# Kernel optimization log

Hardware: AMD Instinct MI355X
Metric: run time of the kernel (lower is better)

## Reference

```python
import jax, jax.numpy as jnp
import numpy as np

D_MODEL = 1024
NUM_HEADS = 16
B, S = 1, 4096


def setup_inputs() -> dict:
    key = jax.random.key(0)
    kx, kq, kk, kv, ko = jax.random.split(key, 5)
    std = (1.0 / D_MODEL) ** 0.5
    def trunc(k):
        return std * jax.random.truncated_normal(k, -3.0, 3.0, (D_MODEL, D_MODEL), dtype=jnp.float32)
    return {
        "x": jax.random.normal(kx, (B, S, D_MODEL), dtype=jnp.float32),
        "W_Q": trunc(kq),
        "W_K": trunc(kk),
        "W_V": trunc(kv),
        "W_O": trunc(ko),
    }


def reference(x, W_Q, W_K, W_V, W_O):
    Bx, Sx, Dm = x.shape
    H = NUM_HEADS
    d_attn = Dm // H
    # projections (torch code uses x @ W.T)
    Q = x @ W_Q.T
    K = x @ W_K.T
    V = x @ W_V.T
    # [B, H, S, d]
    Q = Q.reshape(Bx, Sx, H, d_attn).transpose(0, 2, 1, 3)
    K = K.reshape(Bx, Sx, H, d_attn).transpose(0, 2, 1, 3)
    V = V.reshape(Bx, Sx, H, d_attn).transpose(0, 2, 1, 3)
    scale = 1.0 / jnp.sqrt(jnp.asarray(d_attn, dtype=x.dtype))
    # [B, H, S, S] scores
    attn = jnp.einsum("bhqd,bhkd->bhqk", Q, K) * scale
    causal = jnp.tril(jnp.ones((Sx, Sx), dtype=bool))
    attn = jnp.where(causal, attn, jnp.asarray(-jnp.inf, dtype=attn.dtype))
    probs = jax.nn.softmax(attn, axis=-1)
    y = jnp.einsum("bhqk,bhkd->bhqd", probs, V)
    y = y.transpose(0, 2, 1, 3).reshape(Bx, Sx, Dm)
    return y @ W_O.T
```

## Files before the change

### kernel.cpp

```cpp
#include <hip/hip_runtime.h>

#define S_LEN 4096
#define DMODEL 1024
#define NHEADS 16

typedef __attribute__((ext_vector_type(8))) short bf16x8;
typedef __attribute__((ext_vector_type(4))) float f32x4;
typedef unsigned short u16;
typedef unsigned int u32;
typedef unsigned long long u64;

__device__ inline u16 f2bf(float f) {
    union { float f; u32 u; } v; v.f = f;
    u32 r = v.u + 0x7fffu + ((v.u >> 16) & 1u);
    return (u16)(r >> 16);
}

__device__ inline u32 pkbf2(float a, float b) {
    union { float f; u32 u; } ua, ub; ua.f = a; ub.f = b;
    const u32 ra = ua.u + 0x7fffu + ((ua.u >> 16) & 1u);
    const u32 rb = ub.u + 0x7fffu + ((ub.u >> 16) & 1u);
    return __builtin_amdgcn_perm(rb, ra, 0x07060302u);
}

__device__ inline void cp16(const void* g, void* l) {
    __builtin_amdgcn_global_load_lds(
        (const __attribute__((address_space(1))) unsigned int*)g,
        (__attribute__((address_space(3))) unsigned int*)l, 16, 0, 0);
}

__global__ __launch_bounds__(256) void cvt_all(const float* __restrict__ x,
                                               const float* __restrict__ wq,
                                               const float* __restrict__ wk,
                                               const float* __restrict__ wv,
                                               const float* __restrict__ wo,
                                               u16* __restrict__ xb,
                                               u16* __restrict__ w3,
                                               u16* __restrict__ wob) {
    const int b = blockIdx.x;
    const float* s; u16* d; int off;
    const int NW = DMODEL * DMODEL;
    if (b < 2048)      { s = x;  d = xb;          off = b * 2048; }
    else if (b < 2560) { s = wq; d = w3;          off = (b - 2048) * 2048; }
    else if (b < 3072) { s = wk; d = w3 + NW;     off = (b - 2560) * 2048; }
    else if (b < 3584) { s = wv; d = w3 + 2 * NW; off = (b - 3072) * 2048; }
    else               { s = wo; d = wob;         off = (b - 3584) * 2048; }
    const int i = off + threadIdx.x * 8;
    const float4 a = *(const float4*)(s + i);
    const float4 c = *(const float4*)(s + i + 4);
    u16 t[8];
    t[0] = f2bf(a.x); t[1] = f2bf(a.y); t[2] = f2bf(a.z); t[3] = f2bf(a.w);
    t[4] = f2bf(c.x); t[5] = f2bf(c.y); t[6] = f2bf(c.z); t[7] = f2bf(c.w);
    *(bf16x8*)(d + i) = *(const bf16x8*)t;
}

__global__ __launch_bounds__(256) void gemm_qkv(const u16* __restrict__ A,
                                                const u16* __restrict__ B3,
                                                u16* __restrict__ Qo,
                                                u16* __restrict__ Ko,
                                                u16* __restrict__ Vo) {
    __shared__ __align__(16) u16 As[2][128 * 32];
    __shared__ __align__(16) u16 Bs[2][128 * 32];
    const int tid = threadIdx.x, lane = tid & 63, wave = tid >> 6;
    const int wm = (wave >> 1) * 64, wn = (wave & 1) * 64;
    const int m0 = blockIdx.y * 128, n0 = blockIdx.x * 128;
    const int l15 = lane & 15, quad = lane >> 4;

    f32x4 acc[4][4];
#pragma unroll
    for (int i = 0; i < 4; i++)
#pragma unroll
        for (int j = 0; j < 4; j++) acc[i][j] = (f32x4){0.f, 0.f, 0.f, 0.f};

    const int r0 = tid >> 2, c0 = (tid & 3) * 8;

    cp16(A + (size_t)(m0 + r0) * 1024 + c0,       As[0] + r0 * 32 + c0);
    cp16(A + (size_t)(m0 + r0 + 64) * 1024 + c0,  As[0] + (r0 + 64) * 32 + c0);
    cp16(B3 + (size_t)(n0 + r0) * 1024 + c0,      Bs[0] + r0 * 32 + c0);
    cp16(B3 + (size_t)(n0 + r0 + 64) * 1024 + c0, Bs[0] + (r0 + 64) * 32 + c0);

    int cur = 0;
    for (int kk = 0; kk < 1024; kk += 32) {
        __syncthreads();
        if (kk + 32 < 1024) {
            const int kn = kk + 32;
            cp16(A + (size_t)(m0 + r0) * 1024 + kn + c0,       As[cur ^ 1] + r0 * 32 + c0);
            cp16(A + (size_t)(m0 + r0 + 64) * 1024 + kn + c0,  As[cur ^ 1] + (r0 + 64) * 32 + c0);
            cp16(B3 + (size_t)(n0 + r0) * 1024 + kn + c0,      Bs[cur ^ 1] + r0 * 32 + c0);
            cp16(B3 + (size_t)(n0 + r0 + 64) * 1024 + kn + c0, Bs[cur ^ 1] + (r0 + 64) * 32 + c0);
        }
        bf16x8 af[4], bfr[4];
#pragma unroll
        for (int i = 0; i < 4; i++)
            af[i] = *(const bf16x8*)(As[cur] + (wm + i * 16 + l15) * 32 + quad * 8);
#pragma unroll
        for (int j = 0; j < 4; j++)
            bfr[j] = *(const bf16x8*)(Bs[cur] + (wn + j * 16 + l15) * 32 + quad * 8);
#pragma unroll
        for (int i = 0; i < 4; i++)
#pragma unroll
            for (int j = 0; j < 4; j++)
                acc[i][j] = __builtin_amdgcn_mfma_f32_16x16x32_bf16(af[i], bfr[j], acc[i][j], 0, 0, 0);
        cur ^= 1;
    }

    const int which = n0 >> 10;
    const int n0r = n0 & 1023;
    u16* dst = (which == 0) ? Qo : (which == 1) ? Ko : Vo;
    const float sc = (which == 0) ? 0.125f * 1.4426950408889634f : 1.0f;
#pragma unroll
    for (int i = 0; i < 4; i++)
#pragma unroll
        for (int j = 0; j < 4; j++)
#pragma unroll
            for (int r = 0; r < 4; r++) {
                const int row = m0 + wm + i * 16 + quad * 4 + r;
                const int col = n0r + wn + j * 16 + l15;
                const int h = col >> 6, c = col & 63;
                const u16 v = f2bf(acc[i][j][r] * sc);
                if (which < 2) dst[(size_t)h * S_LEN * 64 + (size_t)row * 64 + c] = v;
                else           dst[(size_t)h * S_LEN * 64 + (size_t)c * S_LEN + row] = v;
            }
}

__global__ __launch_bounds__(256) void gemm_out(const u16* __restrict__ A,
                                                const u16* __restrict__ B,
                                                float* __restrict__ C) {
    __shared__ __align__(16) u16 As[2][64 * 64];
    __shared__ __align__(16) u16 Bs[2][128 * 64];
    const int tid = threadIdx.x, lane = tid & 63, wave = tid >> 6;
    const int wm = (wave >> 1) * 32, wn = (wave & 1) * 64;
    const int bx = blockIdx.x;
    const int n0 = (bx & 7) * 128, m0 = (bx >> 3) * 64;
    const int l15 = lane & 15, quad = lane >> 4;
    const int swz = l15 & 7;

    f32x4 acc[2][4];
#pragma unroll
    for (int i = 0; i < 2; i++)
#pragma unroll
        for (int j = 0; j < 4; j++) acc[i][j] = (f32x4){0.f, 0.f, 0.f, 0.f};

#define STAGE_OUT(buf, kb)                                                              \
    {                                                                                   \
        _Pragma("unroll")                                                               \
        for (int q = 0; q < 2; q++) {                                                   \
            const int ch = tid + q * 256;                                               \
            const int ar = ch >> 3, ac = ((ch & 7) ^ (ar & 7)) * 8;                     \
            cp16(A + (size_t)(m0 + ar) * 1024 + (kb) + ac, As[buf] + ch * 8);           \
        }                                                                               \
        _Pragma("unroll")                                                               \
        for (int q = 0; q < 4; q++) {                                                   \
            const int ch = tid + q * 256;                                               \
            const int br = ch >> 3, bc = ((ch & 7) ^ (br & 7)) * 8;                     \
            cp16(B + (size_t)(n0 + br) * 1024 + (kb) + bc, Bs[buf] + ch * 8);           \
        }                                                                               \
    }

    STAGE_OUT(0, 0);
    int cur = 0;
    for (int kk = 0; kk < 1024; kk += 64) {
        __syncthreads();
        if (kk + 64 < 1024) STAGE_OUT(cur ^ 1, kk + 64);
#pragma unroll
        for (int h = 0; h < 2; h++) {
            const int cc = (h * 4 + quad) ^ swz;
            bf16x8 af[2], bfr[4];
#pragma unroll
            for (int i = 0; i < 2; i++)
                af[i] = *(const bf16x8*)(As[cur] + (wm + i * 16 + l15) * 64 + cc * 8);
#pragma unroll
            for (int j = 0; j < 4; j++)
                bfr[j] = *(const bf16x8*)(Bs[cur] + (wn + j * 16 + l15) * 64 + cc * 8);
#pragma unroll
            for (int i = 0; i < 2; i++)
#pragma unroll
                for (int j = 0; j < 4; j++)
                    acc[i][j] = __builtin_amdgcn_mfma_f32_16x16x32_bf16(af[i], bfr[j], acc[i][j], 0, 0, 0);
        }
        cur ^= 1;
    }
#undef STAGE_OUT

#pragma unroll
    for (int i = 0; i < 2; i++)
#pragma unroll
        for (int j = 0; j < 4; j++)
#pragma unroll
            for (int r = 0; r < 4; r++) {
                const int row = m0 + wm + i * 16 + quad * 4 + r;
                const int col = n0 + wn + j * 16 + l15;
                C[(size_t)row * 1024 + col] = acc[i][j][r];
            }
}

__global__ __launch_bounds__(256) void attn(const u16* __restrict__ Q,
                                            const u16* __restrict__ Kh,
                                            const u16* __restrict__ Vt,
                                            u16* __restrict__ Y) {
    __shared__ __align__(16) u16 Ks[2][64 * 64];
    __shared__ __align__(16) u16 Vs[2][64 * 64];
    __shared__ __align__(16) u16 Pl[4][32 * 72];
    const int b = blockIdx.x;
    const int head = b & 15;
    const int bb = b >> 4;
    const int j = (b < 256) ? bb : 47 - bb;
    const int qaA = 64 * j;
    const int qaB = 64 * (63 - j);
    const int nktB = 64 - j;
    const int tid = threadIdx.x, lane = tid & 63, w = tid >> 6;
    const int l15 = lane & 15, quad = lane >> 4;
    const int swz = l15 & 7;

    const u16* Qp = Q + (size_t)head * S_LEN * 64;
    const u16* Kp = Kh + (size_t)head * S_LEN * 64;
    const u16* Vp = Vt + (size_t)head * 64 * S_LEN;

    const int qrowA = qaA + w * 16 + l15;
    const int qrowB = qaB + w * 16 + l15;
    const int srow = tid >> 3;
    const int scol = ((tid & 7) ^ (srow & 7)) * 8;

    bf16x8 aq[2][2];
#pragma unroll
    for (int s = 0; s < 2; s++) {
        aq[0][s] = *(const bf16x8*)(Qp + (size_t)qrowA * 64 + s * 32 + quad * 8);
        aq[1][s] = *(const bf16x8*)(Qp + (size_t)qrowB * 64 + s * 32 + quad * 8);
    }

    f32x4 o[2][4];
#pragma unroll
    for (int g = 0; g < 2; g++)
#pragma unroll
        for (int jj = 0; jj < 4; jj++) o[g][jj] = (f32x4){0.f, 0.f, 0.f, 0.f};
    float lrow[2] = {0.f, 0.f};

    cp16(Kp + (size_t)srow * 64 + scol,        Ks[0] + tid * 8);
    cp16(Kp + (size_t)(srow + 32) * 64 + scol, Ks[0] + tid * 8 + 2048);
    cp16(Vp + (size_t)srow * S_LEN + scol,        Vs[0] + tid * 8);
    cp16(Vp + (size_t)(srow + 32) * S_LEN + scol, Vs[0] + tid * 8 + 2048);

    int cur = 0;
    for (int kt = 0; kt < nktB; kt++) {
        __syncthreads();
        if (kt + 1 < nktB) {
            const int kn = (kt + 1) * 64;
            cp16(Kp + (size_t)(kn + srow) * 64 + scol,      Ks[cur ^ 1] + tid * 8);
            cp16(Kp + (size_t)(kn + srow + 32) * 64 + scol, Ks[cur ^ 1] + tid * 8 + 2048);
            cp16(Vp + (size_t)srow * S_LEN + kn + scol,        Vs[cur ^ 1] + tid * 8);
            cp16(Vp + (size_t)(srow + 32) * S_LEN + kn + scol, Vs[cur ^ 1] + tid * 8 + 2048);
        }
        const u16* K_ = Ks[cur];
        const u16* V_ = Vs[cur];
        const int kb = kt * 64;
        const bool actA = (kt <= j);
        const bool bndA = (kt == j);
        const bool bndB = (kt == nktB - 1);
#pragma unroll
        for (int t = 0; t < 4; t++) {
            const bf16x8 k0 = *(const bf16x8*)(K_ + (t * 16 + l15) * 64 + (quad ^ swz) * 8);
            const bf16x8 k1 = *(const bf16x8*)(K_ + (t * 16 + l15) * 64 + ((4 + quad) ^ swz) * 8);
            const int keyb = kb + t * 16 + quad * 4;
            {
                f32x4 c = (f32x4){0.f, 0.f, 0.f, 0.f};
                c = __builtin_amdgcn_mfma_f32_16x16x32_bf16(k0, aq[1][0], c, 0, 0, 0);
                c = __builtin_amdgcn_mfma_f32_16x16x32_bf16(k1, aq[1][1], c, 0, 0, 0);
                float p[4];
#pragma unroll
                for (int r = 0; r < 4; r++) {
                    p[r] = exp2f(c[r]);
                    if (bndB && (keyb + r > qrowB)) p[r] = 0.f;
                }
                lrow[1] += (p[0] + p[1]) + (p[2] + p[3]);
                const u32 w0 = pkbf2(p[0], p[1]);
                const u32 w1 = pkbf2(p[2], p[3]);
                *(u64*)(&Pl[w][(16 + l15) * 72 + t * 16 + quad * 4]) =
                    (u64)w0 | ((u64)w1 << 32);
            }
            if (actA) {
                f32x4 c = (f32x4){0.f, 0.f, 0.f, 0.f};
                c = __builtin_amdgcn_mfma_f32_16x16x32_bf16(k0, aq[0][0], c, 0, 0, 0);
                c = __builtin_amdgcn_mfma_f32_16x16x32_bf16(k1, aq[0][1], c, 0, 0, 0);
                float p[4];
#pragma unroll
                for (int r = 0; r < 4; r++) {
                    p[r] = exp2f(c[r]);
                    if (bndA && (keyb + r > qrowA)) p[r] = 0.f;
                }
                lrow[0] += (p[0] + p[1]) + (p[2] + p[3]);
                const u32 w0 = pkbf2(p[0], p[1]);
                const u32 w1 = pkbf2(p[2], p[3]);
                *(u64*)(&Pl[w][l15 * 72 + t * 16 + quad * 4]) =
                    (u64)w0 | ((u64)w1 << 32);
            }
        }
        bf16x8 pB0, pB1, pA0, pA1;
        pB0 = *(const bf16x8*)(&Pl[w][(16 + l15) * 72 + quad * 8]);
        pB1 = *(const bf16x8*)(&Pl[w][(16 + l15) * 72 + 32 + quad * 8]);
        if (actA) {
            pA0 = *(const bf16x8*)(&Pl[w][l15 * 72 + quad * 8]);
            pA1 = *(const bf16x8*)(&Pl[w][l15 * 72 + 32 + quad * 8]);
        }
#pragma unroll
        for (int jj = 0; jj < 4; jj++) {
            const bf16x8 v0 = *(const bf16x8*)(V_ + (jj * 16 + l15) * 64 + (quad ^ swz) * 8);
            const bf16x8 v1 = *(const bf16x8*)(V_ + (jj * 16 + l15) * 64 + ((4 + quad) ^ swz) * 8);
            o[1][jj] = __builtin_amdgcn_mfma_f32_16x16x32_bf16(v0, pB0, o[1][jj], 0, 0, 0);
            o[1][jj] = __builtin_amdgcn_mfma_f32_16x16x32_bf16(v1, pB1, o[1][jj], 0, 0, 0);
            if (actA) {
                o[0][jj] = __builtin_amdgcn_mfma_f32_16x16x32_bf16(v0, pA0, o[0][jj], 0, 0, 0);
                o[0][jj] = __builtin_amdgcn_mfma_f32_16x16x32_bf16(v1, pA1, o[0][jj], 0, 0, 0);
            }
        }
        cur ^= 1;
    }

#pragma unroll
    for (int g = 0; g < 2; g++) {
        lrow[g] += __shfl_xor(lrow[g], 16);
        lrow[g] += __shfl_xor(lrow[g], 32);
        const float inv = 1.f / lrow[g];
        const int qrow = (g == 0) ? qrowA : qrowB;
#pragma unroll
        for (int jj = 0; jj < 4; jj++) {
            const u32 w0 = pkbf2(o[g][jj][0] * inv, o[g][jj][1] * inv);
            const u32 w1 = pkbf2(o[g][jj][2] * inv, o[g][jj][3] * inv);
            *(u64*)(Y + (size_t)qrow * DMODEL + head * 64 + jj * 16 + quad * 4) =
                (u64)w0 | ((u64)w1 << 32);
        }
    }
}

extern "C" void kernel_launch(void* const* d_in, const int* in_sizes, int n_in,
                              void* d_out, int out_size, void* d_ws, size_t ws_size,
                              hipStream_t stream) {
    const float* x  = (const float*)d_in[0];
    const float* wq = (const float*)d_in[1];
    const float* wk = (const float*)d_in[2];
    const float* wv = (const float*)d_in[3];
    const float* wo = (const float*)d_in[4];
    float* out = (float*)d_out;

    u16* qh  = (u16*)d_ws;
    u16* kh  = qh + (size_t)S_LEN * DMODEL;
    u16* vt  = kh + (size_t)S_LEN * DMODEL;
    u16* xb  = vt + (size_t)S_LEN * DMODEL;
    u16* y   = xb;
    u16* wb3 = xb + (size_t)S_LEN * DMODEL;
    u16* wob = wb3 + (size_t)3 * DMODEL * DMODEL;

    const dim3 blk(256);

    cvt_all<<<4096, blk, 0, stream>>>(x, wq, wk, wv, wo, xb, wb3, wob);
    gemm_qkv<<<dim3(3 * DMODEL / 128, S_LEN / 128), blk, 0, stream>>>(xb, wb3, qh, kh, vt);
    attn<<<512, blk, 0, stream>>>(qh, kh, vt, y);
    gemm_out<<<512, blk, 0, stream>>>(y, wob, out);
}
```

Before: 231.0 us.

## Split attention into one q-tile per block with 32-key tiles and 1024 blocks

Result: slower. 244.8 us (+6.0%).

```diff
diff --git a/kernel.cpp b/kernel.cpp
--- a/kernel.cpp
+++ b/kernel.cpp
@@ -198,16 +198,14 @@
                                             const u16* __restrict__ Kh,
                                             const u16* __restrict__ Vt,
                                             u16* __restrict__ Y) {
-    __shared__ __align__(16) u16 Ks[2][64 * 64];
-    __shared__ __align__(16) u16 Vs[2][64 * 64];
-    __shared__ __align__(16) u16 Pl[4][32 * 72];
+    __shared__ __align__(16) u16 Ks[2][32 * 64];
+    __shared__ __align__(16) u16 Vs[2][64 * 32];
+    __shared__ __align__(16) u16 Pl[4][16 * 36];
     const int b = blockIdx.x;
-    const int head = b & 15;
-    const int bb = b >> 4;
-    const int j = (b < 256) ? bb : 47 - bb;
-    const int qaA = 64 * j;
-    const int qaB = 64 * (63 - j);
-    const int nktB = 64 - j;
+    const int i_ = b & 255, k_ = b >> 8;
+    const int head = i_ & 15, s_ = i_ >> 4;
+    const int j = (k_ == 0) ? s_ : (k_ == 1) ? 31 - s_ : (k_ == 2) ? 32 + s_ : 63 - s_;
+    const int nkt = 2 * j + 2;
     const int tid = threadIdx.x, lane = tid & 63, w = tid >> 6;
     const int l15 = lane & 15, quad = lane >> 4;
     const int swz = l15 & 7;
@@ -216,118 +214,80 @@
     const u16* Kp = Kh + (size_t)head * S_LEN * 64;
     const u16* Vp = Vt + (size_t)head * 64 * S_LEN;
 
-    const int qrowA = qaA + w * 16 + l15;
-    const int qrowB = qaB + w * 16 + l15;
-    const int srow = tid >> 3;
-    const int scol = ((tid & 7) ^ (srow & 7)) * 8;
-
-    bf16x8 aq[2][2];
-#pragma unroll
-    for (int s = 0; s < 2; s++) {
-        aq[0][s] = *(const bf16x8*)(Qp + (size_t)qrowA * 64 + s * 32 + quad * 8);
-        aq[1][s] = *(const bf16x8*)(Qp + (size_t)qrowB * 64 + s * 32 + quad * 8);
-    }
-
-    f32x4 o[2][4];
-#pragma unroll
-    for (int g = 0; g < 2; g++)
-#pragma unroll
-        for (int jj = 0; jj < 4; jj++) o[g][jj] = (f32x4){0.f, 0.f, 0.f, 0.f};
-    float lrow[2] = {0.f, 0.f};
-
-    cp16(Kp + (size_t)srow * 64 + scol,        Ks[0] + tid * 8);
-    cp16(Kp + (size_t)(srow + 32) * 64 + scol, Ks[0] + tid * 8 + 2048);
-    cp16(Vp + (size_t)srow * S_LEN + scol,        Vs[0] + tid * 8);
-    cp16(Vp + (size_t)(srow + 32) * S_LEN + scol, Vs[0] + tid * 8 + 2048);
+    const int qbase = 64 * j + w * 16;
+    const int qrow = qbase + l15;
+
+    const int krow = tid >> 3;
+    const int kcol = ((tid & 7) ^ (krow & 7)) * 8;
+    const int vrow = tid >> 2;
+    const int vcol = ((tid & 3) ^ (vrow & 3)) * 8;
+
+    bf16x8 aq[2];
+#pragma unroll
+    for (int s = 0; s < 2; s++)
+        aq[s] = *(const bf16x8*)(Qp + (size_t)qrow * 64 + s * 32 + quad * 8);
+
+    f32x4 o[4];
+#pragma unroll
+    for (int jj = 0; jj < 4; jj++) o[jj] = (f32x4){0.f, 0.f, 0.f, 0.f};
+    float lrow = 0.f;
+
+    cp16(Kp + (size_t)krow * 64 + kcol,   Ks[0] + tid * 8);
+    cp16(Vp + (size_t)vrow * S_LEN + vcol, Vs[0] + tid * 8);
 
     int cur = 0;
-    for (int kt = 0; kt < nktB; kt++) {
+    for (int kt = 0; kt < nkt; kt++) {
         __syncthreads();
-        if (kt + 1 < nktB) {
-            const int kn = (kt + 1) * 64;
-            cp16(Kp + (size_t)(kn + srow) * 64 + scol,      Ks[cur ^ 1] + tid * 8);
-            cp16(Kp + (size_t)(kn + srow + 32) * 64 + scol, Ks[cur ^ 1] + tid * 8 + 2048);
-            cp16(Vp + (size_t)srow * S_LEN + kn + scol,        Vs[cur ^ 1] + tid * 8);
-            cp16(Vp + (size_t)(srow + 32) * S_LEN + kn + scol, Vs[cur ^ 1] + tid * 8 + 2048);
+        if (kt + 1 < nkt) {
+            const int kn = (kt + 1) * 32;
+            cp16(Kp + (size_t)(kn + krow) * 64 + kcol,   Ks[cur ^ 1] + tid * 8);
+            cp16(Vp + (size_t)vrow * S_LEN + kn + vcol,  Vs[cur ^ 1] + tid * 8);
         }
-        const u16* K_ = Ks[cur];
-        const u16* V_ = Vs[cur];
-        const int kb = kt * 64;
-        const bool actA = (kt <= j);
-        const bool bndA = (kt == j);
-        const bool bndB = (kt == nktB - 1);
-#pragma unroll
-        for (int t = 0; t < 4; t++) {
-            const bf16x8 k0 = *(const bf16x8*)(K_ + (t * 16 + l15) * 64 + (quad ^ swz) * 8);
-            const bf16x8 k1 = *(const bf16x8*)(K_ + (t * 16 + l15) * 64 + ((4 + quad) ^ swz) * 8);
-            const int keyb = kb + t * 16 + quad * 4;
-            {
+        const int kb = kt * 32;
+        const bool act = (kb <= qbase + 15);
+        if (act) {
+            const u16* K_ = Ks[cur];
+            const u16* V_ = Vs[cur];
+            const bool bnd = (kb + 31 > qbase);
+#pragma unroll
+            for (int t = 0; t < 2; t++) {
+                const bf16x8 k0 = *(const bf16x8*)(K_ + (t * 16 + l15) * 64 + (quad ^ swz) * 8);
+                const bf16x8 k1 = *(const bf16x8*)(K_ + (t * 16 + l15) * 64 + ((4 + quad) ^ swz) * 8);
                 f32x4 c = (f32x4){0.f, 0.f, 0.f, 0.f};
-                c = __builtin_amdgcn_mfma_f32_16x16x32_bf16(k0, aq[1][0], c, 0, 0, 0);
-                c = __builtin_amdgcn_mfma_f32_16x16x32_bf16(k1, aq[1][1], c, 0, 0, 0);
+                c = __builtin_amdgcn_mfma_f32_16x16x32_bf16(k0, aq[0], c, 0, 0, 0);
+                c = __builtin_amdgcn_mfma_f32_16x16x32_bf16(k1, aq[1], c, 0, 0, 0);
+                const int keyb = kb + t * 16 + quad * 4;
                 float p[4];
 #pragma unroll
                 for (int r = 0; r < 4; r++) {
-                    p[r] = exp2f(c[r]);
-                    if (bndB && (keyb + r > qrowB)) p[r] = 0.f;
+                    p[r] = __builtin_amdgcn_exp2f(c[r]);
+                    if (bnd && (keyb + r > qrow)) p[r] = 0.f;
                 }
-                lrow[1] += (p[0] + p[1]) + (p[2] + p[3]);
+                lrow += (p[0] + p[1]) + (p[2] + p[3]);
                 const u32 w0 = pkbf2(p[0], p[1]);
                 const u32 w1 = pkbf2(p[2], p[3]);
-                *(u64*)(&Pl[w][(16 + l15) * 72 + t * 16 + quad * 4]) =
-                    (u64)w0 | ((u64)w1 << 32);
+                *(u64*)(&Pl[w][l15 * 36 + t * 16 + quad * 4]) = (u64)w0 | ((u64)w1 << 32);
             }
-            if (actA) {
-                f32x4 c = (f32x4){0.f, 0.f, 0.f, 0.f};
-                c = __builtin_amdgcn_mfma_f32_16x16x32_bf16(k0, aq[0][0], c, 0, 0, 0);
-                c = __builtin_amdgcn_mfma_f32_16x16x32_bf16(k1, aq[0][1], c, 0, 0, 0);
-                float p[4];
-#pragma unroll
-                for (int r = 0; r < 4; r++) {
-                    p[r] = exp2f(c[r]);
-                    if (bndA && (keyb + r > qrowA)) p[r] = 0.f;
-                }
-                lrow[0] += (p[0] + p[1]) + (p[2] + p[3]);
-                const u32 w0 = pkbf2(p[0], p[1]);
-                const u32 w1 = pkbf2(p[2], p[3]);
-                *(u64*)(&Pl[w][l15 * 72 + t * 16 + quad * 4]) =
-                    (u64)w0 | ((u64)w1 << 32);
-            }
-        }
-        bf16x8 pB0, pB1, pA0, pA1;
-        pB0 = *(const bf16x8*)(&Pl[w][(16 + l15) * 72 + quad * 8]);
-        pB1 = *(const bf16x8*)(&Pl[w][(16 + l15) * 72 + 32 + quad * 8]);
-        if (actA) {
-            pA0 = *(const bf16x8*)(&Pl[w][l15 * 72 + quad * 8]);
-            pA1 = *(const bf16x8*)(&Pl[w][l15 * 72 + 32 + quad * 8]);
-        }
-#pragma unroll
-        for (int jj = 0; jj < 4; jj++) {
-            const bf16x8 v0 = *(const bf16x8*)(V_ + (jj * 16 + l15) * 64 + (quad ^ swz) * 8);
-            const bf16x8 v1 = *(const bf16x8*)(V_ + (jj * 16 + l15) * 64 + ((4 + quad) ^ swz) * 8);
-            o[1][jj] = __builtin_amdgcn_mfma_f32_16x16x32_bf16(v0, pB0, o[1][jj], 0, 0, 0);
-            o[1][jj] = __builtin_amdgcn_mfma_f32_16x16x32_bf16(v1, pB1, o[1][jj], 0, 0, 0);
-            if (actA) {
-                o[0][jj] = __builtin_amdgcn_mfma_f32_16x16x32_bf16(v0, pA0, o[0][jj], 0, 0, 0);
-                o[0][jj] = __builtin_amdgcn_mfma_f32_16x16x32_bf16(v1, pA1, o[0][jj], 0, 0, 0);
+            const bf16x8 pf = *(const bf16x8*)(&Pl[w][l15 * 36 + quad * 8]);
+#pragma unroll
+            for (int jj = 0; jj < 4; jj++) {
+                const bf16x8 v = *(const bf16x8*)(V_ + (jj * 16 + l15) * 32 +
+                                                  (quad ^ (l15 & 3)) * 8);
+                o[jj] = __builtin_amdgcn_mfma_f32_16x16x32_bf16(v, pf, o[jj], 0, 0, 0);
             }
         }
         cur ^= 1;
     }
 
-#pragma unroll
-    for (int g = 0; g < 2; g++) {
-        lrow[g] += __shfl_xor(lrow[g], 16);
-        lrow[g] += __shfl_xor(lrow[g], 32);
-        const float inv = 1.f / lrow[g];
-        const int qrow = (g == 0) ? qrowA : qrowB;
-#pragma unroll
-        for (int jj = 0; jj < 4; jj++) {
-            const u32 w0 = pkbf2(o[g][jj][0] * inv, o[g][jj][1] * inv);
-            const u32 w1 = pkbf2(o[g][jj][2] * inv, o[g][jj][3] * inv);
-            *(u64*)(Y + (size_t)qrow * DMODEL + head * 64 + jj * 16 + quad * 4) =
-                (u64)w0 | ((u64)w1 << 32);
-        }
+    lrow += __shfl_xor(lrow, 16);
+    lrow += __shfl_xor(lrow, 32);
+    const float inv = 1.f / lrow;
+#pragma unroll
+    for (int jj = 0; jj < 4; jj++) {
+        const u32 w0 = pkbf2(o[jj][0] * inv, o[jj][1] * inv);
+        const u32 w1 = pkbf2(o[jj][2] * inv, o[jj][3] * inv);
+        *(u64*)(Y + (size_t)qrow * DMODEL + head * 64 + jj * 16 + quad * 4) =
+            (u64)w0 | ((u64)w1 << 32);
     }
 }
 
@@ -353,6 +313,6 @@
 
     cvt_all<<<4096, blk, 0, stream>>>(x, wq, wk, wv, wo, xb, wb3, wob);
     gemm_qkv<<<dim3(3 * DMODEL / 128, S_LEN / 128), blk, 0, stream>>>(xb, wb3, qh, kh, vt);
-    attn<<<512, blk, 0, stream>>>(qh, kh, vt, y);
+    attn<<<1024, blk, 0, stream>>>(qh, kh, vt, y);
     gemm_out<<<512, blk, 0, stream>>>(y, wob, out);
 }
```
